# Kernel tuning notes

Hardware: AMD Instinct MI355X
Metric: run time of the kernel (lower is better)

Reference implementation:

```python
import jax, jax.numpy as jnp
import numpy as np

HEADS = 16
DIM_HEAD = 64
SEG = 512        # segment_len (block-diagonal window)
P = 16           # num persistent memory tokens


def rmsnorm(x, g, eps=1e-6):
    var = jnp.mean(x * x, axis=-1, keepdims=True)
    return x * jax.lax.rsqrt(var + eps) * g


def setup_inputs() -> dict:
    key = jax.random.key(0)
    ks = jax.random.split(key, 6)
    B, S, D = 2, 4096, 1024
    inner = HEADS * DIM_HEAD
    return {
        "x": jax.random.normal(ks[0], (B, S, D), jnp.float32),
        "gamma": jnp.ones((D,), jnp.float32),
        "w_qkv": jax.random.normal(ks[1], (D, inner * 3), jnp.float32) * (D ** -0.5),
        "w_out": jax.random.normal(ks[2], (inner, D), jnp.float32) * (inner ** -0.5),
        "pm_k": jax.random.normal(ks[3], (HEADS, P, DIM_HEAD), jnp.float32) * 0.02,
        "pm_v": jax.random.normal(ks[4], (HEADS, P, DIM_HEAD), jnp.float32) * 0.02,
    }


def reference(x, gamma, w_qkv, w_out, pm_k, pm_v):
    # SegmentedAttention forward (MAC block-diagonal causal + persistent memory)
    B, S, D = x.shape
    pad = (-S) % SEG
    Sp = S + pad
    nw = Sp // SEG

    h = rmsnorm(x, gamma)
    qkv = h @ w_qkv                              # [B, S, 3*inner]
    q, k, v = jnp.split(qkv, 3, axis=-1)

    def fold(t):
        # pad and fold segments into batch: b (w n) (h d) -> b w h n d
        t = jnp.pad(t, ((0, 0), (0, pad), (0, 0)))
        t = t.reshape(B, nw, SEG, HEADS, DIM_HEAD)
        return t.transpose(0, 1, 3, 2, 4)        # [B, W, H, SEG, Dh]

    q, k, v = fold(q), fold(k), fold(v)

    # persistent memory tokens prepended to every segment's k/v
    pmk = jnp.broadcast_to(pm_k, (B, nw, HEADS, P, DIM_HEAD))
    pmv = jnp.broadcast_to(pm_v, (B, nw, HEADS, P, DIM_HEAD))
    k = jnp.concatenate([pmk, k], axis=3)        # [B, W, H, P+SEG, Dh]
    v = jnp.concatenate([pmv, v], axis=3)

    scale = DIM_HEAD ** -0.5
    sim = jnp.einsum('bwhid,bwhjd->bwhij', q, k) * scale  # [B,W,H,SEG,P+SEG]

    # mask: persistent mem always visible; within-segment causal (block
    # diagonality is implicit from folding segments into batch)
    qi = jnp.arange(SEG)[:, None]
    kj = jnp.arange(SEG + P)[None, :] - P
    mask = (kj < 0) | (qi >= kj)
    sim = jnp.where(mask, sim, -jnp.inf)

    attn = jax.nn.softmax(sim, axis=-1)
    out = jnp.einsum('bwhij,bwhjd->bwhid', attn, v)       # [B,W,H,SEG,Dh]
    out = out.transpose(0, 1, 3, 2, 4).reshape(B, Sp, HEADS * DIM_HEAD)
    out = out[:, :S]
    return out @ w_out
```

## Files before the change

### kernel.cpp

```cpp
#include <hip/hip_runtime.h>

typedef __attribute__((ext_vector_type(8))) short short8;
typedef __attribute__((ext_vector_type(4))) float float4v;

#define SEG 512
#define PMEM 16
#define NKEY 528

__device__ __forceinline__ float b2f(unsigned int u) {
    union { unsigned int i; float f; } v; v.i = u << 16; return v.f;
}
__device__ __forceinline__ unsigned short f2b(float f) {
    union { float f; unsigned int i; } v; v.f = f;
    unsigned int b = v.i;
    return (unsigned short)((b + 0x7FFFu + ((b >> 16) & 1u)) >> 16);
}

__device__ __forceinline__ void async_ld16(const unsigned short* g, unsigned short* l) {
    __builtin_amdgcn_global_load_lds(
        (const __attribute__((address_space(1))) void*)g,
        (__attribute__((address_space(3))) void*)l,
        16, 0, 0);
}

__global__ void detect_k(const unsigned short* __restrict__ g, int* __restrict__ flag) {
    if (threadIdx.x == 0) {
        int cnt = 0;
        for (int i = 0; i < 64; ++i) cnt += (g[2 * i] == 0x3F80u) ? 1 : 0;
        *flag = (cnt > 48) ? 1 : 0;
    }
}

__global__ void transpose_k(const void* __restrict__ in,
                            unsigned short* __restrict__ out, int R, int C,
                            const int* __restrict__ flagp) {
    __shared__ unsigned short t[32][33];
    int f = flagp[0];
    const unsigned short* in16 = (const unsigned short*)in;
    const float* in32 = (const float*)in;
    int bx = blockIdx.x * 32, by = blockIdx.y * 32;
    int tx = threadIdx.x, ty = threadIdx.y;
    #pragma unroll
    for (int j = 0; j < 32; j += 8) {
        long idx = (long)(by + ty + j) * C + bx + tx;
        t[ty + j][tx] = f ? in16[idx] : f2b(in32[idx]);
    }
    __syncthreads();
    #pragma unroll
    for (int j = 0; j < 32; j += 8)
        out[(long)(bx + ty + j) * R + by + tx] = t[tx][ty + j];
}

__global__ __launch_bounds__(256) void rmsnorm_k(
    const void* __restrict__ xv_, const void* __restrict__ gv_,
    unsigned short* __restrict__ h, const int* __restrict__ flagp) {
    __shared__ float wsum[4];
    int f = flagp[0];
    long row = blockIdx.x;
    int tid = threadIdx.x;
    float f0, f1, f2, f3, g0, g1, g2, g3;
    if (f) {
        const unsigned short* x = (const unsigned short*)xv_;
        const unsigned short* g = (const unsigned short*)gv_;
        uint2 xv = *(const uint2*)(x + row * 1024 + tid * 4);
        f0 = b2f(xv.x & 0xffffu); f1 = b2f(xv.x >> 16);
        f2 = b2f(xv.y & 0xffffu); f3 = b2f(xv.y >> 16);
        uint2 gv = *(const uint2*)(g + tid * 4);
        g0 = b2f(gv.x & 0xffffu); g1 = b2f(gv.x >> 16);
        g2 = b2f(gv.y & 0xffffu); g3 = b2f(gv.y >> 16);
    } else {
        const float* x = (const float*)xv_;
        const float* g = (const float*)gv_;
        float4 xv = *(const float4*)(x + row * 1024 + tid * 4);
        f0 = xv.x; f1 = xv.y; f2 = xv.z; f3 = xv.w;
        float4 gv = *(const float4*)(g + tid * 4);
        g0 = gv.x; g1 = gv.y; g2 = gv.z; g3 = gv.w;
    }
    float ss = f0 * f0 + f1 * f1 + f2 * f2 + f3 * f3;
    #pragma unroll
    for (int off = 1; off < 64; off <<= 1) ss += __shfl_xor(ss, off, 64);
    int lane = tid & 63, wv = tid >> 6;
    if (lane == 0) wsum[wv] = ss;
    __syncthreads();
    float tot = wsum[0] + wsum[1] + wsum[2] + wsum[3];
    float sc = rsqrtf(tot * (1.0f / 1024.0f) + 1e-6f);
    uint2 o;
    o.x = (unsigned int)f2b(f0 * sc * g0) | ((unsigned int)f2b(f1 * sc * g1) << 16);
    o.y = (unsigned int)f2b(f2 * sc * g2) | ((unsigned int)f2b(f3 * sc * g3) << 16);
    *(uint2*)(h + row * 1024 + tid * 4) = o;
}

__global__ __launch_bounds__(256) void gemm_bt(
    const unsigned short* __restrict__ A, const unsigned short* __restrict__ Bt,
    void* __restrict__ Cv, int M, int N, int K,
    const int* __restrict__ flagp, int out_mode) {
    __shared__ unsigned short SM[16384];
    unsigned short* As = SM;
    unsigned short* Bs = SM + 8192;
    int out_bf16 = out_mode == 0 ? 1 : flagp[0];
    int tid = threadIdx.x;
    int lane = tid & 63, wv = tid >> 6;
    int l15 = lane & 15, quad = lane >> 4;
    int wm = (wv >> 1) * 64, wn = (wv & 1) * 64;
    long m0 = (long)blockIdx.y * 128;
    long n0 = (long)blockIdx.x * 128;

    float4v acc[4][4];
    #pragma unroll
    for (int i = 0; i < 4; ++i)
        #pragma unroll
        for (int j = 0; j < 4; ++j) acc[i][j] = (float4v){0.f, 0.f, 0.f, 0.f};

    int r = tid >> 3;
    int c8 = (((tid & 7) ^ (r & 7)) * 8);
    const unsigned short* Ap = A + (m0 + r) * K + c8;
    const unsigned short* Bp = Bt + (n0 + r) * K + c8;
    unsigned short* Ad = As + tid * 8;
    unsigned short* Bd = Bs + tid * 8;

    int s = l15 & 7;

    for (int k0 = 0; k0 < K; k0 += 64) {
        #pragma unroll
        for (int i = 0; i < 4; ++i) {
            async_ld16(Ap + (long)(32 * i) * K + k0, Ad + i * 2048);
            async_ld16(Bp + (long)(32 * i) * K + k0, Bd + i * 2048);
        }
        __syncthreads();
        #pragma unroll
        for (int ksub = 0; ksub < 2; ++ksub) {
            short8 af[4], bfr[4];
            int v = ksub * 4 + quad;
            #pragma unroll
            for (int mt = 0; mt < 4; ++mt)
                af[mt] = *(const short8*)&As[(wm + mt * 16 + l15) * 64 + ((v ^ s) * 8)];
            #pragma unroll
            for (int nt = 0; nt < 4; ++nt)
                bfr[nt] = *(const short8*)&Bs[(wn + nt * 16 + l15) * 64 + ((v ^ s) * 8)];
            #pragma unroll
            for (int mt = 0; mt < 4; ++mt)
                #pragma unroll
                for (int nt = 0; nt < 4; ++nt)
                    acc[mt][nt] = __builtin_amdgcn_mfma_f32_16x16x32_bf16(af[mt], bfr[nt], acc[mt][nt], 0, 0, 0);
        }
        __syncthreads();
    }

    if (out_bf16) {
        unsigned short* Cs = SM;
        #pragma unroll
        for (int mt = 0; mt < 4; ++mt)
            #pragma unroll
            for (int nt = 0; nt < 4; ++nt)
                #pragma unroll
                for (int rr = 0; rr < 4; ++rr) {
                    int row = wm + mt * 16 + quad * 4 + rr;
                    int col = wn + nt * 16 + l15;
                    int colp = col ^ (((row >> 2) & 7) << 4);
                    Cs[row * 128 + colp] = f2b(acc[mt][nt][rr]);
                }
        __syncthreads();
        unsigned short* C = (unsigned short*)Cv;
        #pragma unroll
        for (int p = 0; p < 8; ++p) {
            int off = (p * 256 + tid) * 8;
            int row = off >> 7;
            int colp = off & 127;
            int col = colp ^ (((row >> 2) & 7) << 4);
            *(uint4*)(C + (m0 + row) * N + n0 + col) = *(const uint4*)&Cs[off];
        }
    } else {
        float* Cf = (float*)SM;
        float* C = (float*)Cv;
        #pragma unroll
        for (int half = 0; half < 2; ++half) {
            if (wm == half * 64) {
                #pragma unroll
                for (int mt = 0; mt < 4; ++mt)
                    #pragma unroll
                    for (int nt = 0; nt < 4; ++nt)
                        #pragma unroll
                        for (int rr = 0; rr < 4; ++rr)
                            Cf[(mt * 16 + quad * 4 + rr) * 128 + wn + nt * 16 + l15] = acc[mt][nt][rr];
            }
            __syncthreads();
            #pragma unroll
            for (int p = 0; p < 8; ++p) {
                int off = (p * 256 + tid) * 4;
                int row = off >> 7;
                int col = off & 127;
                *(float4*)(C + (m0 + half * 64 + row) * N + n0 + col) = *(const float4*)&Cf[off];
            }
            __syncthreads();
        }
    }
}

__global__ __launch_bounds__(256) void attn_k(
    const unsigned short* __restrict__ qkv,
    const void* __restrict__ pmk_, const void* __restrict__ pmv_,
    unsigned short* __restrict__ outp, int S, const int* __restrict__ flagp) {
    __shared__ unsigned short Klds[64][72];
    __shared__ unsigned short Vt[64][72];
    __shared__ unsigned short Pbuf[4][16][72];

    int f = flagp[0];
    int hh = blockIdx.x & 15;
    int w  = blockIdx.x >> 4;
    int b  = blockIdx.y;
    int qt = blockIdx.z;

    int tid = threadIdx.x;
    int lane = tid & 63, wv = tid >> 6;
    int l15 = lane & 15, quad = lane >> 4;

    long base_row = (long)b * S + (long)w * SEG;

    int i0 = qt * 64 + wv * 16;
    const unsigned short* qp = qkv + (base_row + i0 + l15) * 3072 + hh * 64;
    short8 aq0 = *(const short8*)(qp + quad * 8);
    short8 aq1 = *(const short8*)(qp + 32 + quad * 8);

    float m_i[4], l_i[4];
    float4v Oacc[4];
    #pragma unroll
    for (int r = 0; r < 4; ++r) { m_i[r] = -1e30f; l_i[r] = 0.f; }
    #pragma unroll
    for (int dt = 0; dt < 4; ++dt) Oacc[dt] = (float4v){0.f, 0.f, 0.f, 0.f};

    const float scale = 0.125f;
    int rot = tid & 7;

    int cmax = qt + 2;
    for (int c = 0; c < cmax; ++c) {
        int jbase = c * 64;
        #pragma unroll
        for (int it = 0; it < 2; ++it) {
            int jl = (tid >> 3) + it * 32;
            int c8 = (tid & 7) * 8;
            int jg = jbase + jl;
            uint4 kd, vd;
            if (c == 0 && jl < PMEM) {
                long off = ((long)hh * PMEM + jl) * 64 + c8;
                if (f) {
                    kd = *(const uint4*)((const unsigned short*)pmk_ + off);
                    vd = *(const uint4*)((const unsigned short*)pmv_ + off);
                } else {
                    const float* pk = (const float*)pmk_ + off;
                    const float* pv = (const float*)pmv_ + off;
                    float4 k0 = *(const float4*)pk, k1 = *(const float4*)(pk + 4);
                    float4 v0 = *(const float4*)pv, v1 = *(const float4*)(pv + 4);
                    kd.x = (unsigned int)f2b(k0.x) | ((unsigned int)f2b(k0.y) << 16);
                    kd.y = (unsigned int)f2b(k0.z) | ((unsigned int)f2b(k0.w) << 16);
                    kd.z = (unsigned int)f2b(k1.x) | ((unsigned int)f2b(k1.y) << 16);
                    kd.w = (unsigned int)f2b(k1.z) | ((unsigned int)f2b(k1.w) << 16);
                    vd.x = (unsigned int)f2b(v0.x) | ((unsigned int)f2b(v0.y) << 16);
                    vd.y = (unsigned int)f2b(v0.z) | ((unsigned int)f2b(v0.w) << 16);
                    vd.z = (unsigned int)f2b(v1.x) | ((unsigned int)f2b(v1.y) << 16);
                    vd.w = (unsigned int)f2b(v1.z) | ((unsigned int)f2b(v1.w) << 16);
                }
            } else if (jg < NKEY) {
                const unsigned short* kp = qkv + (base_row + jg - PMEM) * 3072 + 1024 + hh * 64 + c8;
                kd = *(const uint4*)kp;
                vd = *(const uint4*)(kp + 1024);
            } else {
                kd = (uint4){0, 0, 0, 0};
                vd = (uint4){0, 0, 0, 0};
            }
            *(uint4*)&Klds[jl][c8] = kd;
            union { uint4 u; unsigned short s[8]; } vu; vu.u = vd;
            int colw = (jl + 8 * rot) & 63;
            #pragma unroll
            for (int u = 0; u < 8; ++u) Vt[c8 + u][colw] = vu.s[u];
        }
        __syncthreads();

        float4v sc[4];
        #pragma unroll
        for (int jt = 0; jt < 4; ++jt) {
            float4v a = (float4v){0.f, 0.f, 0.f, 0.f};
            short8 bk0 = *(const short8*)&Klds[jt * 16 + l15][quad * 8];
            short8 bk1 = *(const short8*)&Klds[jt * 16 + l15][32 + quad * 8];
            a = __builtin_amdgcn_mfma_f32_16x16x32_bf16(aq0, bk0, a, 0, 0, 0);
            a = __builtin_amdgcn_mfma_f32_16x16x32_bf16(aq1, bk1, a, 0, 0, 0);
            sc[jt] = a;
        }
        if (c >= qt) {
            #pragma unroll
            for (int jt = 0; jt < 4; ++jt) {
                int jg = jbase + jt * 16 + l15;
                #pragma unroll
                for (int r = 0; r < 4; ++r) {
                    int i = i0 + quad * 4 + r;
                    bool ok = (jg < PMEM) || ((jg < NKEY) && (i >= jg - PMEM));
                    sc[jt][r] = ok ? sc[jt][r] * scale : -1e30f;
                }
            }
        } else {
            #pragma unroll
            for (int jt = 0; jt < 4; ++jt)
                #pragma unroll
                for (int r = 0; r < 4; ++r) sc[jt][r] *= scale;
        }
        #pragma unroll
        for (int r = 0; r < 4; ++r) {
            float tmax = fmaxf(fmaxf(sc[0][r], sc[1][r]), fmaxf(sc[2][r], sc[3][r]));
            #pragma unroll
            for (int off = 1; off < 16; off <<= 1)
                tmax = fmaxf(tmax, __shfl_xor(tmax, off, 64));
            float mnew = fmaxf(m_i[r], tmax);
            float alpha = __expf(m_i[r] - mnew);
            float psum = 0.f;
            #pragma unroll
            for (int jt = 0; jt < 4; ++jt) {
                float p = __expf(sc[jt][r] - mnew);
                sc[jt][r] = p;
                psum += p;
            }
            #pragma unroll
            for (int off = 1; off < 16; off <<= 1)
                psum += __shfl_xor(psum, off, 64);
            l_i[r] = l_i[r] * alpha + psum;
            m_i[r] = mnew;
            #pragma unroll
            for (int dt = 0; dt < 4; ++dt) Oacc[dt][r] *= alpha;
        }
        #pragma unroll
        for (int jt = 0; jt < 4; ++jt)
            #pragma unroll
            for (int r = 0; r < 4; ++r)
                Pbuf[wv][quad * 4 + r][jt * 16 + l15] = f2b(sc[jt][r]);

        short8 ap0 = *(const short8*)&Pbuf[wv][l15][quad * 8];
        short8 ap1 = *(const short8*)&Pbuf[wv][l15][32 + quad * 8];
        #pragma unroll
        for (int dt = 0; dt < 4; ++dt) {
            int d = dt * 16 + l15;
            int cb0 = (quad * 8 + 8 * ((d >> 3) & 7)) & 63;
            int cb1 = (32 + quad * 8 + 8 * ((d >> 3) & 7)) & 63;
            short8 bv0 = *(const short8*)&Vt[d][cb0];
            short8 bv1 = *(const short8*)&Vt[d][cb1];
            Oacc[dt] = __builtin_amdgcn_mfma_f32_16x16x32_bf16(ap0, bv0, Oacc[dt], 0, 0, 0);
            Oacc[dt] = __builtin_amdgcn_mfma_f32_16x16x32_bf16(ap1, bv1, Oacc[dt], 0, 0, 0);
        }
        __syncthreads();
    }

    #pragma unroll
    for (int dt = 0; dt < 4; ++dt)
        #pragma unroll
        for (int r = 0; r < 4; ++r) {
            int i = i0 + quad * 4 + r;
            outp[(base_row + i) * 1024 + hh * 64 + dt * 16 + l15] = f2b(Oacc[dt][r] / l_i[r]);
        }
}

extern "C" void kernel_launch(void* const* d_in, const int* in_sizes, int n_in,
                              void* d_out, int out_size, void* d_ws, size_t ws_size,
                              hipStream_t stream) {
    const void* x     = d_in[0];
    const void* gamma = d_in[1];
    const void* w_qkv = d_in[2];
    const void* w_out = d_in[3];
    const void* pmk   = d_in[4];
    const void* pmv   = d_in[5];

    const int D = 1024, S = 4096;
    const int B = in_sizes[0] / (S * D);
    const long BS = (long)B * S;

    int* flag = (int*)d_ws;
    unsigned short* h     = (unsigned short*)d_ws + 64;
    unsigned short* qkvb  = h + BS * 1024;
    unsigned short* wqkvT = qkvb + BS * 3072;
    unsigned short* woutT = wqkvT + (long)3072 * 1024;
    unsigned short* aout  = h;

    detect_k<<<1, 64, 0, stream>>>((const unsigned short*)gamma, flag);

    dim3 tb(32, 8);
    transpose_k<<<dim3(3072 / 32, 1024 / 32), tb, 0, stream>>>(w_qkv, wqkvT, 1024, 3072, flag);
    transpose_k<<<dim3(1024 / 32, 1024 / 32), tb, 0, stream>>>(w_out, woutT, 1024, 1024, flag);

    rmsnorm_k<<<(int)BS, 256, 0, stream>>>(x, gamma, h, flag);

    gemm_bt<<<dim3(3072 / 128, (int)(BS / 128)), 256, 0, stream>>>(h, wqkvT, qkvb, (int)BS, 3072, 1024, flag, 0);

    attn_k<<<dim3(128, B, 8), 256, 0, stream>>>(qkvb, pmk, pmv, aout, S, flag);

    gemm_bt<<<dim3(1024 / 128, (int)(BS / 128)), 256, 0, stream>>>(aout, woutT, d_out, (int)BS, 1024, 1024, flag, 1);
}
```

Before: 250.6 us.

## Widen attention key tiles to 128, async-load K with swizzle, prescale Q, merge prep kernels

The attention kernel now processes 128 keys per iteration instead of 64, halving the number of barrier/softmax rounds. K tiles are loaded straight into XOR-swizzled LDS with global_load_lds. Q is prescaled by 1/8 once, which removes the per-score scale multiply. The two weight transposes and the persistent-memory bf16 conversion are merged into one prep kernel, removing a launch and the format branch inside attention. Wider tiles raise register and LDS use and add more masked work at the diagonal, and rounding Q after scaling changes numerics slightly.

```diff
diff --git a/kernel.cpp b/kernel.cpp
--- a/kernel.cpp
+++ b/kernel.cpp
@@ -31,24 +31,61 @@
     }
 }
 
-__global__ void transpose_k(const void* __restrict__ in,
-                            unsigned short* __restrict__ out, int R, int C,
-                            const int* __restrict__ flagp) {
-    __shared__ unsigned short t[32][33];
+__global__ __launch_bounds__(256) void prep_k(
+    const void* __restrict__ w_qkv, const void* __restrict__ w_out,
+    const void* __restrict__ pm_k, const void* __restrict__ pm_v,
+    unsigned short* __restrict__ wqkvT, unsigned short* __restrict__ woutT,
+    unsigned short* __restrict__ pmkb, unsigned short* __restrict__ pmvb,
+    const int* __restrict__ flagp) {
     int f = flagp[0];
-    const unsigned short* in16 = (const unsigned short*)in;
-    const float* in32 = (const float*)in;
-    int bx = blockIdx.x * 32, by = blockIdx.y * 32;
-    int tx = threadIdx.x, ty = threadIdx.y;
-    #pragma unroll
-    for (int j = 0; j < 32; j += 8) {
-        long idx = (long)(by + ty + j) * C + bx + tx;
-        t[ty + j][tx] = f ? in16[idx] : f2b(in32[idx]);
-    }
-    __syncthreads();
-    #pragma unroll
-    for (int j = 0; j < 32; j += 8)
-        out[(long)(bx + ty + j) * R + by + tx] = t[tx][ty + j];
+    int bidx = blockIdx.x;
+    int tid = threadIdx.x;
+    if (bidx < 4096) {
+        __shared__ unsigned short t[32][33];
+        const void* in; unsigned short* out; int R, C, bx, by;
+        if (bidx < 3072) {
+            in = w_qkv; out = wqkvT; R = 1024; C = 3072;
+            bx = (bidx % 96) * 32; by = (bidx / 96) * 32;
+        } else {
+            int t2 = bidx - 3072;
+            in = w_out; out = woutT; R = 1024; C = 1024;
+            bx = (t2 & 31) * 32; by = (t2 >> 5) * 32;
+        }
+        const unsigned short* in16 = (const unsigned short*)in;
+        const float* in32 = (const float*)in;
+        int tx = tid & 31, ty = tid >> 5;
+        #pragma unroll
+        for (int j = 0; j < 32; j += 8) {
+            long idx = (long)(by + ty + j) * C + bx + tx;
+            t[ty + j][tx] = f ? in16[idx] : f2b(in32[idx]);
+        }
+        __syncthreads();
+        #pragma unroll
+        for (int j = 0; j < 32; j += 8)
+            out[(long)(bx + ty + j) * R + by + tx] = t[tx][ty + j];
+    } else {
+        int i = (bidx - 4096) * 2048 + tid * 8;
+        if (f) {
+            *(uint4*)(pmkb + i) = *(const uint4*)((const unsigned short*)pm_k + i);
+            *(uint4*)(pmvb + i) = *(const uint4*)((const unsigned short*)pm_v + i);
+        } else {
+            const float* pk = (const float*)pm_k + i;
+            const float* pv = (const float*)pm_v + i;
+            uint4 kd, vd;
+            float4 k0 = *(const float4*)pk, k1 = *(const float4*)(pk + 4);
+            float4 v0 = *(const float4*)pv, v1 = *(const float4*)(pv + 4);
+            kd.x = (unsigned int)f2b(k0.x) | ((unsigned int)f2b(k0.y) << 16);
+            kd.y = (unsigned int)f2b(k0.z) | ((unsigned int)f2b(k0.w) << 16);
+            kd.z = (unsigned int)f2b(k1.x) | ((unsigned int)f2b(k1.y) << 16);
+            kd.w = (unsigned int)f2b(k1.z) | ((unsigned int)f2b(k1.w) << 16);
+            vd.x = (unsigned int)f2b(v0.x) | ((unsigned int)f2b(v0.y) << 16);
+            vd.y = (unsigned int)f2b(v0.z) | ((unsigned int)f2b(v0.w) << 16);
+            vd.z = (unsigned int)f2b(v1.x) | ((unsigned int)f2b(v1.y) << 16);
+            vd.w = (unsigned int)f2b(v1.z) | ((unsigned int)f2b(v1.w) << 16);
+            *(uint4*)(pmkb + i) = kd;
+            *(uint4*)(pmvb + i) = vd;
+        }
+    }
 }
 
 __global__ __launch_bounds__(256) void rmsnorm_k(
@@ -198,13 +235,13 @@
 
 __global__ __launch_bounds__(256) void attn_k(
     const unsigned short* __restrict__ qkv,
-    const void* __restrict__ pmk_, const void* __restrict__ pmv_,
-    unsigned short* __restrict__ outp, int S, const int* __restrict__ flagp) {
-    __shared__ unsigned short Klds[64][72];
-    __shared__ unsigned short Vt[64][72];
-    __shared__ unsigned short Pbuf[4][16][72];
-
-    int f = flagp[0];
+    const unsigned short* __restrict__ pmkb,
+    const unsigned short* __restrict__ pmvb,
+    unsigned short* __restrict__ outp, int S) {
+    __shared__ unsigned short Klds[128 * 64];
+    __shared__ unsigned short Vt[64][136];
+    __shared__ unsigned short Pbuf[4][16][136];
+
     int hh = blockIdx.x & 15;
     int w  = blockIdx.x >> 4;
     int b  = blockIdx.y;
@@ -215,11 +252,16 @@
     int l15 = lane & 15, quad = lane >> 4;
 
     long base_row = (long)b * S + (long)w * SEG;
-
     int i0 = qt * 64 + wv * 16;
+
     const unsigned short* qp = qkv + (base_row + i0 + l15) * 3072 + hh * 64;
     short8 aq0 = *(const short8*)(qp + quad * 8);
     short8 aq1 = *(const short8*)(qp + 32 + quad * 8);
+    #pragma unroll
+    for (int u = 0; u < 8; ++u) {
+        aq0[u] = (short)f2b(b2f((unsigned short)aq0[u]) * 0.125f);
+        aq1[u] = (short)f2b(b2f((unsigned short)aq1[u]) * 0.125f);
+    }
 
     float m_i[4], l_i[4];
     float4v Oacc[4];
@@ -228,83 +270,67 @@
     #pragma unroll
     for (int dt = 0; dt < 4; ++dt) Oacc[dt] = (float4v){0.f, 0.f, 0.f, 0.f};
 
-    const float scale = 0.125f;
+    int jrow = tid >> 3;
+    int cbs = (tid & 7) ^ (jrow & 7);
+    int c8 = (tid & 7) * 8;
     int rot = tid & 7;
 
-    int cmax = qt + 2;
-    for (int c = 0; c < cmax; ++c) {
-        int jbase = c * 64;
-        #pragma unroll
-        for (int it = 0; it < 2; ++it) {
+    int ndc = (qt + 3) >> 1;
+    for (int dc = 0; dc < ndc; ++dc) {
+        #pragma unroll
+        for (int i = 0; i < 4; ++i) {
+            int j = i * 32 + jrow;
+            int jj = dc * 128 + j;
+            const unsigned short* src;
+            if (jj < PMEM)       src = pmkb + ((long)hh * PMEM + jj) * 64 + cbs * 8;
+            else if (jj < NKEY)  src = qkv + (base_row + jj - PMEM) * 3072 + 1024 + hh * 64 + cbs * 8;
+            else                 src = pmkb + cbs * 8;
+            async_ld16(src, Klds + i * 2048 + tid * 8);
+        }
+        #pragma unroll
+        for (int it = 0; it < 4; ++it) {
             int jl = (tid >> 3) + it * 32;
-            int c8 = (tid & 7) * 8;
-            int jg = jbase + jl;
-            uint4 kd, vd;
-            if (c == 0 && jl < PMEM) {
-                long off = ((long)hh * PMEM + jl) * 64 + c8;
-                if (f) {
-                    kd = *(const uint4*)((const unsigned short*)pmk_ + off);
-                    vd = *(const uint4*)((const unsigned short*)pmv_ + off);
-                } else {
-                    const float* pk = (const float*)pmk_ + off;
-                    const float* pv = (const float*)pmv_ + off;
-                    float4 k0 = *(const float4*)pk, k1 = *(const float4*)(pk + 4);
-                    float4 v0 = *(const float4*)pv, v1 = *(const float4*)(pv + 4);
-                    kd.x = (unsigned int)f2b(k0.x) | ((unsigned int)f2b(k0.y) << 16);
-                    kd.y = (unsigned int)f2b(k0.z) | ((unsigned int)f2b(k0.w) << 16);
-                    kd.z = (unsigned int)f2b(k1.x) | ((unsigned int)f2b(k1.y) << 16);
-                    kd.w = (unsigned int)f2b(k1.z) | ((unsigned int)f2b(k1.w) << 16);
-                    vd.x = (unsigned int)f2b(v0.x) | ((unsigned int)f2b(v0.y) << 16);
-                    vd.y = (unsigned int)f2b(v0.z) | ((unsigned int)f2b(v0.w) << 16);
-                    vd.z = (unsigned int)f2b(v1.x) | ((unsigned int)f2b(v1.y) << 16);
-                    vd.w = (unsigned int)f2b(v1.z) | ((unsigned int)f2b(v1.w) << 16);
-                }
-            } else if (jg < NKEY) {
-                const unsigned short* kp = qkv + (base_row + jg - PMEM) * 3072 + 1024 + hh * 64 + c8;
-                kd = *(const uint4*)kp;
-                vd = *(const uint4*)(kp + 1024);
-            } else {
-                kd = (uint4){0, 0, 0, 0};
-                vd = (uint4){0, 0, 0, 0};
-            }
-            *(uint4*)&Klds[jl][c8] = kd;
+            int jj = dc * 128 + jl;
+            uint4 vd;
+            if (jj < PMEM)      vd = *(const uint4*)(pmvb + ((long)hh * PMEM + jj) * 64 + c8);
+            else if (jj < NKEY) vd = *(const uint4*)(qkv + (base_row + jj - PMEM) * 3072 + 2048 + hh * 64 + c8);
+            else                vd = (uint4){0, 0, 0, 0};
             union { uint4 u; unsigned short s[8]; } vu; vu.u = vd;
-            int colw = (jl + 8 * rot) & 63;
+            int half = jl >> 6, jl6 = jl & 63;
+            int colw = ((jl6 + 8 * rot) & 63) + (half << 6);
             #pragma unroll
             for (int u = 0; u < 8; ++u) Vt[c8 + u][colw] = vu.s[u];
         }
         __syncthreads();
 
-        float4v sc[4];
-        #pragma unroll
-        for (int jt = 0; jt < 4; ++jt) {
+        float4v sc[8];
+        #pragma unroll
+        for (int jt = 0; jt < 8; ++jt) {
+            int j = jt * 16 + l15;
+            int sw = j & 7;
+            short8 bk0 = *(const short8*)&Klds[j * 64 + ((quad ^ sw) * 8)];
+            short8 bk1 = *(const short8*)&Klds[j * 64 + (((quad + 4) ^ sw) * 8)];
             float4v a = (float4v){0.f, 0.f, 0.f, 0.f};
-            short8 bk0 = *(const short8*)&Klds[jt * 16 + l15][quad * 8];
-            short8 bk1 = *(const short8*)&Klds[jt * 16 + l15][32 + quad * 8];
             a = __builtin_amdgcn_mfma_f32_16x16x32_bf16(aq0, bk0, a, 0, 0, 0);
             a = __builtin_amdgcn_mfma_f32_16x16x32_bf16(aq1, bk1, a, 0, 0, 0);
             sc[jt] = a;
         }
-        if (c >= qt) {
-            #pragma unroll
-            for (int jt = 0; jt < 4; ++jt) {
-                int jg = jbase + jt * 16 + l15;
+        if (dc * 128 + 112 > qt * 64) {
+            #pragma unroll
+            for (int jt = 0; jt < 8; ++jt) {
+                int jg = dc * 128 + jt * 16 + l15;
                 #pragma unroll
                 for (int r = 0; r < 4; ++r) {
                     int i = i0 + quad * 4 + r;
                     bool ok = (jg < PMEM) || ((jg < NKEY) && (i >= jg - PMEM));
-                    sc[jt][r] = ok ? sc[jt][r] * scale : -1e30f;
+                    sc[jt][r] = ok ? sc[jt][r] : -1e30f;
                 }
             }
-        } else {
-            #pragma unroll
-            for (int jt = 0; jt < 4; ++jt)
-                #pragma unroll
-                for (int r = 0; r < 4; ++r) sc[jt][r] *= scale;
         }
         #pragma unroll
         for (int r = 0; r < 4; ++r) {
-            float tmax = fmaxf(fmaxf(sc[0][r], sc[1][r]), fmaxf(sc[2][r], sc[3][r]));
+            float tmax = fmaxf(fmaxf(fmaxf(sc[0][r], sc[1][r]), fmaxf(sc[2][r], sc[3][r])),
+                               fmaxf(fmaxf(sc[4][r], sc[5][r]), fmaxf(sc[6][r], sc[7][r])));
             #pragma unroll
             for (int off = 1; off < 16; off <<= 1)
                 tmax = fmaxf(tmax, __shfl_xor(tmax, off, 64));
@@ -312,7 +338,7 @@
             float alpha = __expf(m_i[r] - mnew);
             float psum = 0.f;
             #pragma unroll
-            for (int jt = 0; jt < 4; ++jt) {
+            for (int jt = 0; jt < 8; ++jt) {
                 float p = __expf(sc[jt][r] - mnew);
                 sc[jt][r] = p;
                 psum += p;
@@ -326,22 +352,28 @@
             for (int dt = 0; dt < 4; ++dt) Oacc[dt][r] *= alpha;
         }
         #pragma unroll
-        for (int jt = 0; jt < 4; ++jt)
+        for (int jt = 0; jt < 8; ++jt)
             #pragma unroll
             for (int r = 0; r < 4; ++r)
                 Pbuf[wv][quad * 4 + r][jt * 16 + l15] = f2b(sc[jt][r]);
 
-        short8 ap0 = *(const short8*)&Pbuf[wv][l15][quad * 8];
-        short8 ap1 = *(const short8*)&Pbuf[wv][l15][32 + quad * 8];
+        short8 ap[4];
+        #pragma unroll
+        for (int kt = 0; kt < 4; ++kt)
+            ap[kt] = *(const short8*)&Pbuf[wv][l15][kt * 32 + quad * 8];
+
         #pragma unroll
         for (int dt = 0; dt < 4; ++dt) {
             int d = dt * 16 + l15;
-            int cb0 = (quad * 8 + 8 * ((d >> 3) & 7)) & 63;
-            int cb1 = (32 + quad * 8 + 8 * ((d >> 3) & 7)) & 63;
-            short8 bv0 = *(const short8*)&Vt[d][cb0];
-            short8 bv1 = *(const short8*)&Vt[d][cb1];
-            Oacc[dt] = __builtin_amdgcn_mfma_f32_16x16x32_bf16(ap0, bv0, Oacc[dt], 0, 0, 0);
-            Oacc[dt] = __builtin_amdgcn_mfma_f32_16x16x32_bf16(ap1, bv1, Oacc[dt], 0, 0, 0);
+            int rb = (d >> 3) & 7;
+            #pragma unroll
+            for (int kt = 0; kt < 4; ++kt) {
+                int k0b = kt * 32 + quad * 8;
+                int half = k0b >> 6, j6 = k0b & 63;
+                int col = ((j6 + rb * 8) & 63) + (half << 6);
+                short8 bv = *(const short8*)&Vt[d][col];
+                Oacc[dt] = __builtin_amdgcn_mfma_f32_16x16x32_bf16(ap[kt], bv, Oacc[dt], 0, 0, 0);
+            }
         }
         __syncthreads();
     }
@@ -374,19 +406,19 @@
     unsigned short* qkvb  = h + BS * 1024;
     unsigned short* wqkvT = qkvb + BS * 3072;
     unsigned short* woutT = wqkvT + (long)3072 * 1024;
+    unsigned short* pmkb  = woutT + (long)1024 * 1024;
+    unsigned short* pmvb  = pmkb + 16384;
     unsigned short* aout  = h;
 
     detect_k<<<1, 64, 0, stream>>>((const unsigned short*)gamma, flag);
 
-    dim3 tb(32, 8);
-    transpose_k<<<dim3(3072 / 32, 1024 / 32), tb, 0, stream>>>(w_qkv, wqkvT, 1024, 3072, flag);
-    transpose_k<<<dim3(1024 / 32, 1024 / 32), tb, 0, stream>>>(w_out, woutT, 1024, 1024, flag);
+    prep_k<<<4104, 256, 0, stream>>>(w_qkv, w_out, pmk, pmv, wqkvT, woutT, pmkb, pmvb, flag);
 
     rmsnorm_k<<<(int)BS, 256, 0, stream>>>(x, gamma, h, flag);
 
     gemm_bt<<<dim3(3072 / 128, (int)(BS / 128)), 256, 0, stream>>>(h, wqkvT, qkvb, (int)BS, 3072, 1024, flag, 0);
 
-    attn_k<<<dim3(128, B, 8), 256, 0, stream>>>(qkvb, pmk, pmv, aout, S, flag);
+    attn_k<<<dim3(128, B, 8), 256, 0, stream>>>(qkvb, pmkb, pmvb, aout, S);
 
     gemm_bt<<<dim3(1024 / 128, (int)(BS / 128)), 256, 0, stream>>>(aout, woutT, d_out, (int)BS, 1024, 1024, flag, 1);
 }
```

New measurement: 248.1 us. No clear change (-1.0%).
